# Kernel optimization log

Measured on AMD Instinct MI355X. Metric: run time of the kernel, lower is better.

The kernel has to match this reference:

```python
import jax, jax.numpy as jnp
import numpy as np

N_U = 50000; N_I = 50000; DIM = 64; NNZ = 2_000_000; Q = 5
LAYERS = 2; B = 1024; P = 10; NNEG = 40
MARGIN = 0.5; LAMBDA1 = 0.2; BATCH_USER = 1024


def setup_inputs() -> dict:
    key = jax.random.key(0)
    ks = jax.random.split(key, 12)
    return {
        "E_u_0": jax.random.normal(ks[0], (N_U, DIM), jnp.float32) * 0.1,
        "E_i_0": jax.random.normal(ks[1], (N_I, DIM), jnp.float32) * 0.1,
        "vals": jax.random.uniform(ks[2], (NNZ,), jnp.float32) * 0.05,  # normalized adj values
        "u_mul_s": jax.random.normal(ks[3], (N_U, Q), jnp.float32) * 0.1,
        "vt": jax.random.normal(ks[4], (Q, N_I), jnp.float32) * 0.1,
        "v_mul_s": jax.random.normal(ks[5], (N_I, Q), jnp.float32) * 0.1,
        "ut": jax.random.normal(ks[6], (Q, N_U), jnp.float32) * 0.1,
        "rows": jax.random.randint(ks[7], (NNZ,), 0, N_U, jnp.int32),
        "cols": jax.random.randint(ks[8], (NNZ,), 0, N_I, jnp.int32),
        "uids": jax.random.randint(ks[9], (B,), 0, N_U, jnp.int32),
        "pos": jax.random.randint(ks[10], (B, P), 0, N_I, jnp.int32),
        "neg": jax.random.randint(ks[11], (B, NNEG), 0, N_I, jnp.int32),
    }


def _leaky(x):
    return jnp.where(x > 0, x, 0.5 * x)  # LeakyReLU(0.5)


def reference(E_u_0, E_i_0, vals, u_mul_s, vt, v_mul_s, ut, rows, cols, uids, pos, neg):
    # --- GCN propagation (dropout=0 -> sparse_dropout is identity) ---
    E_u, E_i = E_u_0, E_i_0
    sum_u, sum_i = E_u_0, E_i_0
    for _ in range(LAYERS):
        # spmm(adj, E_i): out[r] += val * E_i[c]
        Z_du = _leaky(jax.ops.segment_sum(vals[:, None] * E_i[cols], rows, num_segments=N_U))
        # spmm(adj.T, E_u): out[c] += val * E_u[r]
        Z_di = _leaky(jax.ops.segment_sum(vals[:, None] * E_u[rows], cols, num_segments=N_I))
        # SVD hyper-conv (computed in original forward; unused by returned loss)
        G_u = _leaky(u_mul_s @ (vt @ E_i))
        G_i = _leaky(v_mul_s @ (ut @ E_u))
        del G_u, G_i
        E_u, E_i = Z_du + E_u, Z_di + E_i
        sum_u, sum_i = sum_u + E_u, sum_i + E_i

    # --- U_IConstLoss, vectorized over the original per-uid Python loop ---
    u_emb = sum_u[uids]                                  # [B, D]
    pos_emb = sum_i[pos]                                 # [B, P, D]
    neg_emb = sum_i[neg]                                 # [B, N, D]
    pos_scores = jnp.einsum("bd,bpd->bp", u_emb, pos_emb)
    neg_scores = jnp.einsum("bd,bnd->bn", u_emb, neg_emb)
    # pos_d = score at argmin == min; neg_d = score at argmax == max
    pos_d = pos_scores.min(axis=1)
    neg_d = neg_scores.max(axis=1)
    delta = jnp.where(neg_d - pos_d > 0.005, 10.0 * (pos_d - neg_d), 0.0)
    # loss_d accumulates across the loop and the running value is added each iter
    loss_d_cum = jnp.cumsum(delta)
    pos_hinge = jax.nn.relu(1.0 - pos_scores).sum(axis=1)          # sum over P
    neg_hinge = jax.nn.relu(neg_scores - MARGIN).sum(axis=1)       # scalar per user
    bpr_sum = pos_hinge + P * neg_hinge                            # bpr.sum() per user
    loss_r = (bpr_sum.sum() + loss_d_cum.sum()) / BATCH_USER
    loss = loss_r + LAMBDA1
    return loss
```

## Files before the change

### kernel.cpp

```cpp
#include <hip/hip_runtime.h>

#define N_U   50000
#define N_I   50000
#define NSEG  (N_U + N_I)
#define DIM   64
#define B_USERS 1024
#define P_POS 10
#define N_NEG 40

#define BSEG  128
#define NBUK  782
#define CAP   8192
#define EPB   4096
#define TPAD  16

#ifndef __has_builtin
#define __has_builtin(x) 0
#endif
#if __has_builtin(__builtin_amdgcn_cvt_pk_f32_fp8) && __has_builtin(__builtin_amdgcn_cvt_pk_fp8_f32)
#define HAVE_FP8 1
#else
#define HAVE_FP8 0
#endif

typedef float f32x2 __attribute__((ext_vector_type(2)));

__device__ __forceinline__ unsigned f2b(float f) {
    unsigned b = __float_as_uint(f);
    return (b + 0x7FFFu + ((b >> 16) & 1u)) >> 16;
}
__device__ __forceinline__ float b2f(unsigned u) {
    return __uint_as_float(u << 16);
}
__device__ __forceinline__ float blo(unsigned u) { return __uint_as_float(u << 16); }
__device__ __forceinline__ float bhi(unsigned u) { return __uint_as_float(u & 0xFFFF0000u); }

#if !HAVE_FP8
__device__ __forceinline__ float dec8(unsigned v) {
    unsigned s = (v >> 7) & 1u, ef = (v >> 3) & 0xFu, m = v & 7u;
    float r = (ef == 0u) ? (float)m * 0.001953125f
                         : __uint_as_float(((ef + 120u) << 23) | (m << 20));
    return s ? -r : r;
}
__device__ __forceinline__ unsigned enc8(float f) {
    unsigned b = __float_as_uint(f);
    unsigned s = b >> 31;
    float a = fabsf(f);
    if (a >= 448.f) return (s << 7) | 0x7Eu;
    if (a < 0.015625f) return s << 7;
    int e = (int)((b >> 23) & 0xFF) - 120;
    unsigned m = b & 0x7FFFFFu;
    unsigned keep = m >> 20, rem = m & 0xFFFFFu;
    keep += (rem > 0x80000u) || (rem == 0x80000u && (keep & 1u));
    if (keep == 8u) { keep = 0u; ++e; if (e > 15) return (s << 7) | 0x7Eu; }
    if (e == 15 && keep == 7u) keep = 6u;
    return (s << 7) | ((unsigned)e << 3) | keep;
}
#endif

__device__ __forceinline__ void dec4v(unsigned u, f32x2& p01, f32x2& p23) {
#if HAVE_FP8
    p01 = __builtin_amdgcn_cvt_pk_f32_fp8((int)u, false);
    p23 = __builtin_amdgcn_cvt_pk_f32_fp8((int)u, true);
#else
    p01.x = dec8(u & 0xFFu); p01.y = dec8((u >> 8) & 0xFFu);
    p23.x = dec8((u >> 16) & 0xFFu); p23.y = dec8(u >> 24);
#endif
}
__device__ __forceinline__ unsigned enc4(float f0, float f1, float f2, float f3) {
#if HAVE_FP8
    int w = 0;
    w = __builtin_amdgcn_cvt_pk_fp8_f32(f0, f1, w, false);
    w = __builtin_amdgcn_cvt_pk_fp8_f32(f2, f3, w, true);
    return (unsigned)w;
#else
    return enc8(f0) | (enc8(f1) << 8) | (enc8(f2) << 16) | (enc8(f3) << 24);
#endif
}

__device__ __forceinline__ void pkfma(f32x2& a, f32x2 b, f32x2 c) {
    asm("v_pk_fma_f32 %0, %1, %2, %0" : "+v"(a) : "v"(b), "v"(c));
}
__device__ __forceinline__ void pkadd(f32x2& a, f32x2 t) {
    asm("v_pk_add_f32 %0, %0, %1" : "+v"(a) : "v"(t));
}

__global__ void k_conv(const float* __restrict__ Eu0, const float* __restrict__ Ei0,
                       ushort* __restrict__ E0b, unsigned* __restrict__ E0f8) {
    int p = blockIdx.x * blockDim.x + threadIdx.x;
    if (p >= NSEG * (DIM / 4)) return;
    float4 v = (p < N_U * (DIM / 4)) ? ((const float4*)Eu0)[p]
                                     : ((const float4*)Ei0)[p - N_U * (DIM / 4)];
    ushort4 o;
    o.x = (ushort)f2b(v.x); o.y = (ushort)f2b(v.y);
    o.z = (ushort)f2b(v.z); o.w = (ushort)f2b(v.w);
    ((ushort4*)E0b)[p] = o;
    E0f8[p] = enc4(v.x, v.y, v.z, v.w);
}

__global__ __launch_bounds__(512) void k_binA(const float* __restrict__ vals,
                                              const int* __restrict__ rows,
                                              const int* __restrict__ cols,
                                              int* __restrict__ tails,
                                              uint2* __restrict__ stage, int nnz) {
    __shared__ int hist[1024];
    __shared__ int cur[NBUK];
    __shared__ int adj[NBUK];
    __shared__ uint2 srt[2 * EPB];
    int t = threadIdx.x;
    hist[t] = 0; hist[t + 512] = 0;
    __syncthreads();

    int e0 = blockIdx.x * EPB;
    int rem = nnz - e0;
    int ne = rem < EPB ? rem : EPB;
    int nrec = 2 * ne;

    for (int k = t; k < ne; k += 512) {
        int e = e0 + k;
        atomicAdd(&hist[rows[e] >> 7], 1);
        atomicAdd(&hist[(N_U + cols[e]) >> 7], 1);
    }
    __syncthreads();

    int v0 = hist[t], v1 = hist[t + 512];
    for (int o = 1; o < 1024; o <<= 1) {
        int x0 = (t >= o) ? hist[t - o] : 0;
        int x1 = (t + 512 >= o) ? hist[t + 512 - o] : 0;
        __syncthreads();
        hist[t] += x0; hist[t + 512] += x1;
        __syncthreads();
    }
    {
        int i0 = t, i1 = t + 512;
        int l0 = hist[i0] - v0, l1 = hist[i1] - v1;
        if (i0 < NBUK) {
            cur[i0] = l0;
            adj[i0] = (v0 ? atomicAdd(&tails[i0 * TPAD], v0) : 0) - l0;
        }
        if (i1 < NBUK) {
            cur[i1] = l1;
            adj[i1] = (v1 ? atomicAdd(&tails[i1 * TPAD], v1) : 0) - l1;
        }
    }
    __syncthreads();

    for (int k = t; k < ne; k += 512) {
        int e = e0 + k;
        int r = rows[e];
        int g = N_U + cols[e];
        unsigned b = __float_as_uint(vals[e]);
        unsigned v15 = ((b + 0x7FFFu + ((b >> 16) & 1u)) >> 16) & 0x7FFFu;
        int b0 = r >> 7;
        int rk0 = atomicAdd(&cur[b0], 1);
        uint2 s0; s0.x = (((unsigned)g) << 15) | v15;
        s0.y = ((unsigned)b0 << 7) | (unsigned)(r & 127);
        srt[rk0] = s0;
        int b1 = g >> 7;
        int rk1 = atomicAdd(&cur[b1], 1);
        uint2 s1; s1.x = (((unsigned)r) << 15) | v15;
        s1.y = ((unsigned)b1 << 7) | (unsigned)(g & 127);
        srt[rk1] = s1;
    }
    __syncthreads();

    for (int i = t; i < nrec; i += 512) {
        uint2 s = srt[i];
        int bkt = s.y >> 7;
        int slot = i + adj[bkt];
        if (slot < CAP) {
            uint2 rec; rec.x = s.x; rec.y = s.y & 127u;
            stage[((size_t)bkt << 13) + slot] = rec;
        }
    }
}

__global__ __launch_bounds__(1024) void k_bscan(const int* __restrict__ tails,
                                                int* __restrict__ bukoff) {
    __shared__ int sh[1024];
    int t = threadIdx.x;
    int v = (t < NBUK) ? min(tails[t * TPAD], CAP) : 0;
    sh[t] = v;
    __syncthreads();
    for (int o = 1; o < 1024; o <<= 1) {
        int x = (t >= o) ? sh[t - o] : 0;
        __syncthreads();
        sh[t] += x;
        __syncthreads();
    }
    if (t < NBUK) bukoff[t] = sh[t] - v;
}

__global__ __launch_bounds__(256) void k_binB2(const uint2* __restrict__ stage,
                                               const int* __restrict__ tails,
                                               const int* __restrict__ bukoff,
                                               unsigned* __restrict__ edges,
                                               int* __restrict__ cnt,
                                               int* __restrict__ endo) {
    __shared__ int h[BSEG];
    __shared__ int sc[BSEG];
    __shared__ int cur[BSEG];
    int b = blockIdx.x, t = threadIdx.x;
    int cs = min(tails[b * TPAD], CAP);
    size_t sbase = (size_t)b << 13;
    if (t < BSEG) h[t] = 0;
    __syncthreads();
    for (int i = t; i < cs; i += 256)
        atomicAdd(&h[stage[sbase + i].y], 1);
    __syncthreads();
    if (t < BSEG) sc[t] = h[t];
    __syncthreads();
    for (int o = 1; o < BSEG; o <<= 1) {
        int x = (t < BSEG && t >= o) ? sc[t - o] : 0;
        __syncthreads();
        if (t < BSEG) sc[t] += x;
        __syncthreads();
    }
    int seg0 = b * BSEG;
    if (t < BSEG) {
        int start = bukoff[b] + sc[t] - h[t];
        cur[t] = start;
        int seg = seg0 + t;
        if (seg < NSEG) { cnt[seg] = h[t]; endo[seg] = start + h[t]; }
    }
    __syncthreads();
    for (int i = t; i < cs; i += 256) {
        uint2 rec = stage[sbase + i];
        int pos = atomicAdd(&cur[rec.y], 1);
        edges[pos] = rec.x;
    }
}

template <int WF8>
__global__ __launch_bounds__(256) void k_prop(const unsigned* __restrict__ edges,
                                              const int* __restrict__ endo,
                                              const int* __restrict__ cnt,
                                              const ushort* __restrict__ Ecur,
                                              const unsigned* __restrict__ F8cur,
                                              ushort* __restrict__ Enext,
                                              unsigned* __restrict__ F8next) {
    int sid  = (blockIdx.x * blockDim.x + threadIdx.x) >> 5;
    int lane = threadIdx.x & 63;
    if (sid >= NSEG) return;
    int l32  = lane & 31;
    int hbase = lane & 32;
    int qq   = l32 >> 3;
    int l7   = lane & 7;
    int end = endo[sid], n = cnt[sid], start = end - n;

    f32x2 a0 = {0.f, 0.f}, a1 = {0.f, 0.f}, a2 = {0.f, 0.f}, a3 = {0.f, 0.f};
    for (int b = 0; b < n; b += 32) {
        int k = b + l32;
        unsigned pk = (k < n) ? edges[start + k] : 0u;
        int m = min(n - b, 32);
        for (int j = 0; j < m; j += 4) {
            int sel = j + qq;
            unsigned pj = __shfl(pk, hbase + sel, 64);
            float v = (sel < m) ? __uint_as_float((pj & 0x7FFFu) << 16) : 0.0f;
            unsigned idx = pj >> 15;
            uint2 ev = *(const uint2*)(F8cur + (size_t)idx * 16 + l7 * 2);
            f32x2 e01, e23, e45, e67;
            dec4v(ev.x, e01, e23);
            dec4v(ev.y, e45, e67);
            f32x2 vv = {v, v};
            pkfma(a0, vv, e01);
            pkfma(a1, vv, e23);
            pkfma(a2, vv, e45);
            pkfma(a3, vv, e67);
        }
    }
    #pragma unroll
    for (int off = 8; off <= 16; off <<= 1) {
        f32x2 t;
        t.x = __shfl_xor(a0.x, off, 64); t.y = __shfl_xor(a0.y, off, 64); pkadd(a0, t);
        t.x = __shfl_xor(a1.x, off, 64); t.y = __shfl_xor(a1.y, off, 64); pkadd(a1, t);
        t.x = __shfl_xor(a2.x, off, 64); t.y = __shfl_xor(a2.y, off, 64); pkadd(a2, t);
        t.x = __shfl_xor(a3.x, off, 64); t.y = __shfl_xor(a3.y, off, 64); pkadd(a3, t);
    }
    if (qq == 0) {
        uint4 ec = ((const uint4*)(Ecur + (size_t)sid * DIM))[l7];
        float r0 = blo(ec.x) + (a0.x > 0.f ? a0.x : 0.5f * a0.x);
        float r1 = bhi(ec.x) + (a0.y > 0.f ? a0.y : 0.5f * a0.y);
        float r2 = blo(ec.y) + (a1.x > 0.f ? a1.x : 0.5f * a1.x);
        float r3 = bhi(ec.y) + (a1.y > 0.f ? a1.y : 0.5f * a1.y);
        float r4 = blo(ec.z) + (a2.x > 0.f ? a2.x : 0.5f * a2.x);
        float r5 = bhi(ec.z) + (a2.y > 0.f ? a2.y : 0.5f * a2.y);
        float r6 = blo(ec.w) + (a3.x > 0.f ? a3.x : 0.5f * a3.x);
        float r7 = bhi(ec.w) + (a3.y > 0.f ? a3.y : 0.5f * a3.y);
        uint4 o;
        o.x = f2b(r0) | (f2b(r1) << 16);
        o.y = f2b(r2) | (f2b(r3) << 16);
        o.z = f2b(r4) | (f2b(r5) << 16);
        o.w = f2b(r6) | (f2b(r7) << 16);
        ((uint4*)(Enext + (size_t)sid * DIM))[l7] = o;
        if (WF8) {
            uint2 st;
            st.x = enc4(r0, r1, r2, r3);
            st.y = enc4(r4, r5, r6, r7);
            *(uint2*)(F8next + (size_t)sid * 16 + l7 * 2) = st;
        }
    }
}

__global__ __launch_bounds__(256) void k_loss(const ushort* __restrict__ E0,
                                              const ushort* __restrict__ E1,
                                              const ushort* __restrict__ E2,
                                              const int* __restrict__ uids,
                                              const int* __restrict__ pos,
                                              const int* __restrict__ neg,
                                              float* __restrict__ acc) {
    int wid  = (blockIdx.x * blockDim.x + threadIdx.x) >> 6;
    int lane = threadIdx.x & 63;
    if (wid >= B_USERS) return;

    int uid = uids[wid];
    size_t ub = (size_t)uid * DIM + lane;
    float u = b2f(E0[ub]) + b2f(E1[ub]) + b2f(E2[ub]);

    float pos_min = 1e30f, pos_h = 0.0f;
    for (int p = 0; p < P_POS; ++p) {
        int it = pos[wid * P_POS + p];
        size_t ib = (size_t)(N_U + it) * DIM + lane;
        float si = b2f(E0[ib]) + b2f(E1[ib]) + b2f(E2[ib]);
        float s = u * si;
        #pragma unroll
        for (int o = 32; o > 0; o >>= 1) s += __shfl_xor(s, o, 64);
        pos_min = fminf(pos_min, s);
        pos_h  += fmaxf(1.0f - s, 0.0f);
    }

    float neg_max = -1e30f, neg_h = 0.0f;
    for (int nn = 0; nn < N_NEG; ++nn) {
        int it = neg[wid * N_NEG + nn];
        size_t ib = (size_t)(N_U + it) * DIM + lane;
        float si = b2f(E0[ib]) + b2f(E1[ib]) + b2f(E2[ib]);
        float s = u * si;
        #pragma unroll
        for (int o = 32; o > 0; o >>= 1) s += __shfl_xor(s, o, 64);
        neg_max = fmaxf(neg_max, s);
        neg_h  += fmaxf(s - 0.5f, 0.0f);
    }

    float delta = (neg_max - pos_min > 0.005f) ? 10.0f * (pos_min - neg_max) : 0.0f;
    float contrib = pos_h + (float)P_POS * neg_h + delta * (float)(B_USERS - wid);
    if (lane == 0) atomicAdd(acc, contrib);
}

__global__ void finalize(const float* __restrict__ acc, float* __restrict__ out) {
    out[0] = acc[0] / (float)B_USERS + 0.2f;
}

extern "C" void kernel_launch(void* const* d_in, const int* in_sizes, int n_in,
                              void* d_out, int out_size, void* d_ws, size_t ws_size,
                              hipStream_t stream) {
    const float* Eu0  = (const float*)d_in[0];
    const float* Ei0  = (const float*)d_in[1];
    const float* vals = (const float*)d_in[2];
    const int* rows = (const int*)d_in[7];
    const int* cols = (const int*)d_in[8];
    const int* uids = (const int*)d_in[9];
    const int* pos  = (const int*)d_in[10];
    const int* neg  = (const int*)d_in[11];
    int nnz = in_sizes[2];

    unsigned* edges  = (unsigned*)d_ws;
    uint2*    stage  = (uint2*)(edges + (size_t)2 * nnz);
    ushort*   E0b    = (ushort*)(stage + (size_t)NBUK * CAP);
    ushort*   E1b    = E0b + (size_t)NSEG * DIM;
    ushort*   E2b    = E1b + (size_t)NSEG * DIM;
    unsigned* E0f8   = (unsigned*)(E2b + (size_t)NSEG * DIM);
    unsigned* E1f8   = E0f8 + (size_t)NSEG * 16;
    int*      cnt    = (int*)(E1f8 + (size_t)NSEG * 16);
    int*      endo   = cnt + NSEG;
    int*      bukoff = endo + NSEG;
    int*      tails  = bukoff + NBUK;
    float*    acc    = (float*)(tails + NBUK * TPAD);

    const int blk = 256;

    hipMemsetAsync(tails, 0, (NBUK * TPAD + 1) * sizeof(int), stream);

    k_conv<<<(NSEG * (DIM / 4) + blk - 1) / blk, blk, 0, stream>>>(Eu0, Ei0, E0b, E0f8);
    k_binA<<<(nnz + EPB - 1) / EPB, 512, 0, stream>>>(vals, rows, cols, tails, stage, nnz);
    k_bscan<<<1, 1024, 0, stream>>>(tails, bukoff);
    k_binB2<<<NBUK, blk, 0, stream>>>(stage, tails, bukoff, edges, cnt, endo);

    const int prop_blocks = (NSEG * 32 + blk - 1) / blk;
    k_prop<1><<<prop_blocks, blk, 0, stream>>>(edges, endo, cnt, E0b, E0f8, E1b, E1f8);
    k_prop<0><<<prop_blocks, blk, 0, stream>>>(edges, endo, cnt, E1b, E1f8, E2b, nullptr);

    k_loss<<<(B_USERS * 64) / blk, blk, 0, stream>>>(E0b, E1b, E2b, uids, pos, neg, acc);
    finalize<<<1, 1, 0, stream>>>(acc, (float*)d_out);
}
```

Before: 227.1 us.

## Fold bucket scan into binB2, fuse finalize into loss, unroll prop loop

Removes the single-block bucket prefix-scan kernel: each binB2 block now reduces the tails of all earlier buckets itself to get its output offset. The finalize kernel is folded into k_loss with a last-block-done counter that writes the final scalar. The k_prop inner gather loop drops its per-iteration bounds check, which is safe because out-of-range lanes hold a zero packed record and so contribute weight 0, and it is unrolled by 2. The aim is fewer kernel launches and serial gaps, at the cost of redundant tail reads in every binB2 block and an extra atomic counter.

```diff
diff --git a/kernel.cpp b/kernel.cpp
--- a/kernel.cpp
+++ b/kernel.cpp
@@ -175,32 +175,27 @@
     }
 }
 
-__global__ __launch_bounds__(1024) void k_bscan(const int* __restrict__ tails,
-                                                int* __restrict__ bukoff) {
-    __shared__ int sh[1024];
-    int t = threadIdx.x;
-    int v = (t < NBUK) ? min(tails[t * TPAD], CAP) : 0;
-    sh[t] = v;
-    __syncthreads();
-    for (int o = 1; o < 1024; o <<= 1) {
-        int x = (t >= o) ? sh[t - o] : 0;
-        __syncthreads();
-        sh[t] += x;
-        __syncthreads();
-    }
-    if (t < NBUK) bukoff[t] = sh[t] - v;
-}
-
 __global__ __launch_bounds__(256) void k_binB2(const uint2* __restrict__ stage,
                                                const int* __restrict__ tails,
-                                               const int* __restrict__ bukoff,
                                                unsigned* __restrict__ edges,
                                                int* __restrict__ cnt,
                                                int* __restrict__ endo) {
+    __shared__ int red[256];
     __shared__ int h[BSEG];
     __shared__ int sc[BSEG];
     __shared__ int cur[BSEG];
     int b = blockIdx.x, t = threadIdx.x;
+
+    int part = 0;
+    for (int i = t; i < b; i += 256) part += min(tails[i * TPAD], CAP);
+    red[t] = part;
+    __syncthreads();
+    for (int o = 128; o > 0; o >>= 1) {
+        if (t < o) red[t] += red[t + o];
+        __syncthreads();
+    }
+    int bukoff_b = red[0];
+
     int cs = min(tails[b * TPAD], CAP);
     size_t sbase = (size_t)b << 13;
     if (t < BSEG) h[t] = 0;
@@ -218,7 +213,7 @@
     }
     int seg0 = b * BSEG;
     if (t < BSEG) {
-        int start = bukoff[b] + sc[t] - h[t];
+        int start = bukoff_b + sc[t] - h[t];
         cur[t] = start;
         int seg = seg0 + t;
         if (seg < NSEG) { cnt[seg] = h[t]; endo[seg] = start + h[t]; }
@@ -253,10 +248,10 @@
         int k = b + l32;
         unsigned pk = (k < n) ? edges[start + k] : 0u;
         int m = min(n - b, 32);
+        #pragma unroll 2
         for (int j = 0; j < m; j += 4) {
-            int sel = j + qq;
-            unsigned pj = __shfl(pk, hbase + sel, 64);
-            float v = (sel < m) ? __uint_as_float((pj & 0x7FFFu) << 16) : 0.0f;
+            unsigned pj = __shfl(pk, hbase + j + qq, 64);
+            float v = __uint_as_float((pj & 0x7FFFu) << 16);
             unsigned idx = pj >> 15;
             uint2 ev = *(const uint2*)(F8cur + (size_t)idx * 16 + l7 * 2);
             f32x2 e01, e23, e45, e67;
@@ -308,46 +303,53 @@
                                               const int* __restrict__ uids,
                                               const int* __restrict__ pos,
                                               const int* __restrict__ neg,
-                                              float* __restrict__ acc) {
+                                              float* __restrict__ acc,
+                                              int* __restrict__ done,
+                                              float* __restrict__ out) {
     int wid  = (blockIdx.x * blockDim.x + threadIdx.x) >> 6;
     int lane = threadIdx.x & 63;
-    if (wid >= B_USERS) return;
-
-    int uid = uids[wid];
-    size_t ub = (size_t)uid * DIM + lane;
-    float u = b2f(E0[ub]) + b2f(E1[ub]) + b2f(E2[ub]);
-
-    float pos_min = 1e30f, pos_h = 0.0f;
-    for (int p = 0; p < P_POS; ++p) {
-        int it = pos[wid * P_POS + p];
-        size_t ib = (size_t)(N_U + it) * DIM + lane;
-        float si = b2f(E0[ib]) + b2f(E1[ib]) + b2f(E2[ib]);
-        float s = u * si;
-        #pragma unroll
-        for (int o = 32; o > 0; o >>= 1) s += __shfl_xor(s, o, 64);
-        pos_min = fminf(pos_min, s);
-        pos_h  += fmaxf(1.0f - s, 0.0f);
-    }
-
-    float neg_max = -1e30f, neg_h = 0.0f;
-    for (int nn = 0; nn < N_NEG; ++nn) {
-        int it = neg[wid * N_NEG + nn];
-        size_t ib = (size_t)(N_U + it) * DIM + lane;
-        float si = b2f(E0[ib]) + b2f(E1[ib]) + b2f(E2[ib]);
-        float s = u * si;
-        #pragma unroll
-        for (int o = 32; o > 0; o >>= 1) s += __shfl_xor(s, o, 64);
-        neg_max = fmaxf(neg_max, s);
-        neg_h  += fmaxf(s - 0.5f, 0.0f);
-    }
-
-    float delta = (neg_max - pos_min > 0.005f) ? 10.0f * (pos_min - neg_max) : 0.0f;
-    float contrib = pos_h + (float)P_POS * neg_h + delta * (float)(B_USERS - wid);
-    if (lane == 0) atomicAdd(acc, contrib);
-}
-
-__global__ void finalize(const float* __restrict__ acc, float* __restrict__ out) {
-    out[0] = acc[0] / (float)B_USERS + 0.2f;
+    if (wid < B_USERS) {
+        int uid = uids[wid];
+        size_t ub = (size_t)uid * DIM + lane;
+        float u = b2f(E0[ub]) + b2f(E1[ub]) + b2f(E2[ub]);
+
+        float pos_min = 1e30f, pos_h = 0.0f;
+        for (int p = 0; p < P_POS; ++p) {
+            int it = pos[wid * P_POS + p];
+            size_t ib = (size_t)(N_U + it) * DIM + lane;
+            float si = b2f(E0[ib]) + b2f(E1[ib]) + b2f(E2[ib]);
+            float s = u * si;
+            #pragma unroll
+            for (int o = 32; o > 0; o >>= 1) s += __shfl_xor(s, o, 64);
+            pos_min = fminf(pos_min, s);
+            pos_h  += fmaxf(1.0f - s, 0.0f);
+        }
+
+        float neg_max = -1e30f, neg_h = 0.0f;
+        for (int nn = 0; nn < N_NEG; ++nn) {
+            int it = neg[wid * N_NEG + nn];
+            size_t ib = (size_t)(N_U + it) * DIM + lane;
+            float si = b2f(E0[ib]) + b2f(E1[ib]) + b2f(E2[ib]);
+            float s = u * si;
+            #pragma unroll
+            for (int o = 32; o > 0; o >>= 1) s += __shfl_xor(s, o, 64);
+            neg_max = fmaxf(neg_max, s);
+            neg_h  += fmaxf(s - 0.5f, 0.0f);
+        }
+
+        float delta = (neg_max - pos_min > 0.005f) ? 10.0f * (pos_min - neg_max) : 0.0f;
+        float contrib = pos_h + (float)P_POS * neg_h + delta * (float)(B_USERS - wid);
+        if (lane == 0) atomicAdd(acc, contrib);
+    }
+    __syncthreads();
+    if (threadIdx.x == 0) {
+        __threadfence();
+        int old = atomicAdd(done, 1);
+        if (old == (int)gridDim.x - 1) {
+            float a = atomicAdd(acc, 0.0f);
+            out[0] = a / (float)B_USERS + 0.2f;
+        }
+    }
 }
 
 extern "C" void kernel_launch(void* const* d_in, const int* in_sizes, int n_in,
@@ -372,23 +374,22 @@
     unsigned* E1f8   = E0f8 + (size_t)NSEG * 16;
     int*      cnt    = (int*)(E1f8 + (size_t)NSEG * 16);
     int*      endo   = cnt + NSEG;
-    int*      bukoff = endo + NSEG;
-    int*      tails  = bukoff + NBUK;
+    int*      tails  = endo + NSEG;
     float*    acc    = (float*)(tails + NBUK * TPAD);
+    int*      done   = (int*)(acc + 1);
 
     const int blk = 256;
 
-    hipMemsetAsync(tails, 0, (NBUK * TPAD + 1) * sizeof(int), stream);
+    hipMemsetAsync(tails, 0, (NBUK * TPAD + 2) * sizeof(int), stream);
 
     k_conv<<<(NSEG * (DIM / 4) + blk - 1) / blk, blk, 0, stream>>>(Eu0, Ei0, E0b, E0f8);
     k_binA<<<(nnz + EPB - 1) / EPB, 512, 0, stream>>>(vals, rows, cols, tails, stage, nnz);
-    k_bscan<<<1, 1024, 0, stream>>>(tails, bukoff);
-    k_binB2<<<NBUK, blk, 0, stream>>>(stage, tails, bukoff, edges, cnt, endo);
+    k_binB2<<<NBUK, blk, 0, stream>>>(stage, tails, edges, cnt, endo);
 
     const int prop_blocks = (NSEG * 32 + blk - 1) / blk;
     k_prop<1><<<prop_blocks, blk, 0, stream>>>(edges, endo, cnt, E0b, E0f8, E1b, E1f8);
     k_prop<0><<<prop_blocks, blk, 0, stream>>>(edges, endo, cnt, E1b, E1f8, E2b, nullptr);
 
-    k_loss<<<(B_USERS * 64) / blk, blk, 0, stream>>>(E0b, E1b, E2b, uids, pos, neg, acc);
-    finalize<<<1, 1, 0, stream>>>(acc, (float*)d_out);
-}
+    k_loss<<<(B_USERS * 64) / blk, blk, 0, stream>>>(E0b, E1b, E2b, uids, pos, neg,
+                                                     acc, done, (float*)d_out);
+}
```

Result: no change. 225.5 us (-0.7%).
